# Kernel optimization log

Hardware: AMD Instinct MI355X
Metric: run time of the kernel (lower is better)

The kernel has to match this reference:

```python
import jax, jax.numpy as jnp
import numpy as np

C = 512
GROUPS = 32
EPS = 1e-6


def group_norm(x, w, b):
    # x: [B, C, H, W]
    B, Cc, H, W = x.shape
    xg = x.reshape(B, GROUPS, Cc // GROUPS, H, W)
    mean = xg.mean(axis=(2, 3, 4), keepdims=True)
    var = xg.var(axis=(2, 3, 4), keepdims=True)
    xg = (xg - mean) * jax.lax.rsqrt(var + EPS)
    x = xg.reshape(B, Cc, H, W)
    return x * w[None, :, None, None] + b[None, :, None, None]


def conv1x1(x, w, b):
    # 1x1 conv == per-pixel channel matmul; w: [Cout, Cin]
    return jnp.einsum('bchw,oc->bohw', x, w) + b[None, :, None, None]


def setup_inputs() -> dict:
    key = jax.random.key(0)
    ks = jax.random.split(key, 11)
    s = 1.0 / np.sqrt(C)
    d = {
        'x': jax.random.normal(ks[0], (2, C, 64, 64), dtype=jnp.float32),
        'gn_w': jnp.ones((C,), jnp.float32),
        'gn_b': jnp.zeros((C,), jnp.float32),
        'wq': jax.random.normal(ks[1], (C, C), jnp.float32) * s,
        'bq': jax.random.normal(ks[2], (C,), jnp.float32) * 0.01,
        'wk': jax.random.normal(ks[3], (C, C), jnp.float32) * s,
        'bk': jax.random.normal(ks[4], (C,), jnp.float32) * 0.01,
        'wv': jax.random.normal(ks[5], (C, C), jnp.float32) * s,
        'bv': jax.random.normal(ks[6], (C,), jnp.float32) * 0.01,
        'wo': jax.random.normal(ks[7], (C, C), jnp.float32) * s,
        'bo': jax.random.normal(ks[8], (C,), jnp.float32) * 0.01,
    }
    return d


def reference(x, gn_w, gn_b, wq, bq, wk, bk, wv, bv, wo, bo):
    B, Cc, H, W = x.shape
    h = group_norm(x, gn_w, gn_b)
    q = conv1x1(h, wq, bq)  # [B,C,H,W]
    k = conv1x1(h, wk, bk)
    v = conv1x1(h, wv, bv)
    N = H * W
    q = q.reshape(B, Cc, N).transpose(0, 2, 1)   # b n c
    k = k.reshape(B, Cc, N)                      # b c n
    v = v.reshape(B, Cc, N)                      # b c n
    attn = jnp.einsum('bic,bcj->bij', q, k) * (Cc ** -0.5)  # [B,N,N]
    attn = jax.nn.softmax(attn, axis=-1)
    # h_[b,c,i] = sum_j v[b,c,j] * attn[b,i,j]
    h_ = jnp.einsum('bcj,bij->bci', v, attn).reshape(B, Cc, H, W)
    h_ = conv1x1(h_, wo, bo)
    return x + h_
```

## Files before the change

### kernel.cpp

```cpp
#include <hip/hip_runtime.h>


typedef __attribute__((ext_vector_type(8))) short bf16x8;
typedef __attribute__((ext_vector_type(4))) float f32x4;
typedef unsigned short u16;
typedef unsigned int u32;

__device__ __forceinline__ u16 f2bf(float f) {
  u32 u = __builtin_bit_cast(u32, f);
  return (u16)((u + 0x7FFFu + ((u >> 16) & 1u)) >> 16);
}
__device__ __forceinline__ float bf2f(u16 u) {
  return __builtin_bit_cast(float, (u32)u << 16);
}
__device__ __forceinline__ void gll16(const void* g, void* l) {
  __builtin_amdgcn_global_load_lds((const __attribute__((address_space(1))) u32*)g,
                                   (__attribute__((address_space(3))) u32*)l, 16, 0, 0);
}

__global__ void zero_stats(float* __restrict__ stats) {
  if (threadIdx.x < 128) stats[threadIdx.x] = 0.f;
}

__global__ __launch_bounds__(256) void gn_stats(const float* __restrict__ x,
                                                float* __restrict__ stats) {
  int bg = blockIdx.x >> 3, slice = blockIdx.x & 7;
  const float4* xp = (const float4*)(x + (size_t)bg * 65536 + slice * 8192);
  int t = threadIdx.x;
  float s = 0.f, ss = 0.f;
  for (int i = t; i < 2048; i += 256) {
    float4 v = xp[i];
    s += v.x + v.y + v.z + v.w;
    ss += v.x * v.x + v.y * v.y + v.z * v.z + v.w * v.w;
  }
  for (int off = 32; off > 0; off >>= 1) {
    s += __shfl_down(s, off);
    ss += __shfl_down(ss, off);
  }
  __shared__ float rs[4], rss[4];
  if ((t & 63) == 0) { rs[t >> 6] = s; rss[t >> 6] = ss; }
  __syncthreads();
  if (t == 0) {
    atomicAdd(&stats[bg * 2 + 0], rs[0] + rs[1] + rs[2] + rs[3]);
    atomicAdd(&stats[bg * 2 + 1], rss[0] + rss[1] + rss[2] + rss[3]);
  }
}

__global__ __launch_bounds__(256) void gn_apply(
    const float* __restrict__ x, const float* __restrict__ w,
    const float* __restrict__ b, const float* __restrict__ stats,
    u16* __restrict__ ht) {
  int bg = blockIdx.x >> 3, slice = blockIdx.x & 7;
  int batch = bg >> 5, g = bg & 31;
  const float* xp = x + (size_t)bg * 65536;
  float mean = stats[bg * 2 + 0] * (1.f / 65536.f);
  float var = stats[bg * 2 + 1] * (1.f / 65536.f) - mean * mean;
  float rstd = rsqrtf(var + 1e-6f);
  float wsc[16], bsc[16];
#pragma unroll
  for (int cc = 0; cc < 16; ++cc) {
    float wv = w[g * 16 + cc];
    wsc[cc] = wv * rstd;
    bsc[cc] = b[g * 16 + cc] - mean * wsc[cc];
  }
  u16* hp = ht + (size_t)batch * 4096 * 512 + g * 16;
  int t = threadIdx.x;
  for (int n = slice * 512 + t; n < slice * 512 + 512; n += 256) {
    union { u16 pk[16]; uint4 v4[2]; } u;
#pragma unroll
    for (int cc = 0; cc < 16; ++cc)
      u.pk[cc] = f2bf(xp[cc * 4096 + n] * wsc[cc] + bsc[cc]);
    uint4* dst = (uint4*)(hp + (size_t)n * 512);
    dst[0] = u.v4[0];
    dst[1] = u.v4[1];
  }
}

__global__ __launch_bounds__(256) void wcvt_kernel(
    const float* __restrict__ wq, const float* __restrict__ wk,
    const float* __restrict__ wv, const float* __restrict__ wo,
    const float* __restrict__ bq, const float* __restrict__ bk,
    u16* __restrict__ Wqk, u16* __restrict__ Wv, u16* __restrict__ Wo,
    float* __restrict__ Bqk) {
  int i = blockIdx.x * 256 + threadIdx.x;
  Wqk[i] = f2bf(wq[i]);
  Wqk[262144 + i] = f2bf(wk[i]);
  Wv[i] = f2bf(wv[i]);
  Wo[i] = f2bf(wo[i]);
  if (i < 512) { Bqk[i] = bq[i]; Bqk[512 + i] = bk[i]; }
}

template <int BM, int BN, int MODE>
__global__ __launch_bounds__(256) void mfma_gemm(
    const u16* __restrict__ A, int sA, const u16* __restrict__ B, int sB,
    int K, const float* __restrict__ bias, const float* __restrict__ res,
    void* __restrict__ out, int ostr, float scale) {
  constexpr int TM = BM / 32, TN = BN / 32;
  constexpr int SIA = BM / 32, SIB = BN / 32;
  __shared__ char sm[(BM + BN) * 128];
  char* As = sm;
  char* Bs = sm + BM * 128;
  int t = threadIdx.x;
  int w = t >> 6, lane = t & 63, quad = lane >> 4, ln = lane & 15;
  int wm = w >> 1, wn = w & 1;
  int m0 = blockIdx.y * BM, n0 = blockIdx.x * BN;
  f32x4 acc[TM][TN] = {};

  for (int k0 = 0; k0 < K; k0 += 64) {
#pragma unroll
    for (int si = 0; si < SIA; ++si) {
      int s = (w * SIA + si) * 64 + lane;
      gll16(A + (size_t)(m0 + (s & (BM - 1))) * sA + k0 + (s / BM) * 8,
            As + (w * SIA + si) * 1024);
    }
#pragma unroll
    for (int si = 0; si < SIB; ++si) {
      int s = (w * SIB + si) * 64 + lane;
      gll16(B + (size_t)(n0 + (s & (BN - 1))) * sB + k0 + (s / BN) * 8,
            Bs + (w * SIB + si) * 1024);
    }
    __syncthreads();
#pragma unroll
    for (int ks = 0; ks < 2; ++ks) {
      bf16x8 af[TM], bfr[TN];
#pragma unroll
      for (int tm = 0; tm < TM; ++tm)
        af[tm] = *(const bf16x8*)(As + (((ks * 4 + quad) * BM) + wm * (BM / 2) + tm * 16 + ln) * 16);
#pragma unroll
      for (int tn = 0; tn < TN; ++tn)
        bfr[tn] = *(const bf16x8*)(Bs + (((ks * 4 + quad) * BN) + wn * (BN / 2) + tn * 16 + ln) * 16);
#pragma unroll
      for (int tm = 0; tm < TM; ++tm)
#pragma unroll
        for (int tn = 0; tn < TN; ++tn)
          acc[tm][tn] = __builtin_amdgcn_mfma_f32_16x16x32_bf16(af[tm], bfr[tn], acc[tm][tn], 0, 0, 0);
    }
    __syncthreads();
  }

#pragma unroll
  for (int tm = 0; tm < TM; ++tm) {
    int mb = m0 + wm * (BM / 2) + tm * 16 + quad * 4;
#pragma unroll
    for (int tn = 0; tn < TN; ++tn) {
      int n = n0 + wn * (BN / 2) + tn * 16 + ln;
      float bn = (MODE == 0) ? bias[n] : 0.f;
#pragma unroll
      for (int r = 0; r < 4; ++r) {
        int m = mb + r;
        float v = acc[tm][tn][r];
        if (MODE == 0) {
          ((u16*)out)[(size_t)m * ostr + n] = f2bf(v + bn);
        } else if (MODE == 1) {
          ((u16*)out)[(size_t)m * ostr + n] = f2bf(v + bias[m]);
        } else if (MODE == 2) {
          int bb = n >> 12, nn = n & 4095;
          size_t off = ((size_t)(bb * 512 + m)) * 4096 + nn;
          ((float*)out)[off] = v + bias[m] + res[off];
        } else if (MODE == 3) {
          ((u16*)out)[(size_t)m * ostr + n] = f2bf(v * scale);
        } else {
          ((u16*)out)[(size_t)m * ostr + n] = f2bf(v);
        }
      }
    }
  }
}

__global__ __launch_bounds__(256) void softmax_kernel(u16* __restrict__ S) {
  u16* sp = S + (size_t)blockIdx.x * 4096;
  int t = threadIdx.x;
  int w = t >> 6;
  uint4 a = ((const uint4*)sp)[t * 2];
  uint4 b = ((const uint4*)sp)[t * 2 + 1];
  u32 words[8] = {a.x, a.y, a.z, a.w, b.x, b.y, b.z, b.w};
  float v[16];
#pragma unroll
  for (int i = 0; i < 8; ++i) {
    v[2 * i] = bf2f((u16)(words[i] & 0xFFFF));
    v[2 * i + 1] = bf2f((u16)(words[i] >> 16));
  }
  float mx = v[0];
#pragma unroll
  for (int i = 1; i < 16; ++i) mx = fmaxf(mx, v[i]);
#pragma unroll
  for (int d = 1; d < 64; d <<= 1) mx = fmaxf(mx, __shfl_xor(mx, d));
  __shared__ float red[8];
  if ((t & 63) == 0) red[w] = mx;
  __syncthreads();
  mx = fmaxf(fmaxf(red[0], red[1]), fmaxf(red[2], red[3]));
  float sum = 0.f;
#pragma unroll
  for (int i = 0; i < 16; ++i) {
    v[i] = __expf(v[i] - mx);
    sum += v[i];
  }
#pragma unroll
  for (int d = 1; d < 64; d <<= 1) sum += __shfl_xor(sum, d);
  if ((t & 63) == 0) red[4 + w] = sum;
  __syncthreads();
  float inv = 1.f / (red[4] + red[5] + red[6] + red[7]);
#pragma unroll
  for (int i = 0; i < 8; ++i)
    words[i] = (u32)f2bf(v[2 * i] * inv) | ((u32)f2bf(v[2 * i + 1] * inv) << 16);
  ((uint4*)sp)[t * 2] = make_uint4(words[0], words[1], words[2], words[3]);
  ((uint4*)sp)[t * 2 + 1] = make_uint4(words[4], words[5], words[6], words[7]);
}

extern "C" void kernel_launch(void* const* d_in, const int* in_sizes, int n_in,
                              void* d_out, int out_size, void* d_ws, size_t ws_size,
                              hipStream_t stream) {
  (void)in_sizes; (void)n_in; (void)out_size; (void)ws_size;
  const float* x = (const float*)d_in[0];
  const float* gnw = (const float*)d_in[1];
  const float* gnb = (const float*)d_in[2];
  const float* wq = (const float*)d_in[3];
  const float* bq = (const float*)d_in[4];
  const float* wk = (const float*)d_in[5];
  const float* bk = (const float*)d_in[6];
  const float* wv = (const float*)d_in[7];
  const float* bv = (const float*)d_in[8];
  const float* wo = (const float*)d_in[9];
  const float* bo = (const float*)d_in[10];
  float* out = (float*)d_out;

  char* ws = (char*)d_ws;
  u16* ht  = (u16*)(ws);
  u16* AOt = (u16*)(ws);
  u16* QKt = (u16*)(ws + 8388608);
  u16* S   = (u16*)(ws + 25165824);
  u16* Wqk = (u16*)(ws + 58720256);
  u16* Wv  = (u16*)(ws + 59768832);
  u16* Wo  = (u16*)(ws + 60293120);
  u16* Vg      = (u16*)d_out;
  float* stats = (float*)((char*)d_out + 8388608);
  float* Bqk   = (float*)((char*)d_out + 8389120);

  wcvt_kernel<<<1024, 256, 0, stream>>>(wq, wk, wv, wo, bq, bk, Wqk, Wv, Wo, Bqk);
  zero_stats<<<1, 128, 0, stream>>>(stats);
  gn_stats<<<512, 256, 0, stream>>>(x, stats);
  gn_apply<<<512, 256, 0, stream>>>(x, gnw, gnb, stats, ht);
  mfma_gemm<128, 128, 0><<<dim3(8, 64), 256, 0, stream>>>(
      ht, 512, Wqk, 512, 512, Bqk, nullptr, QKt, 1024, 1.f);
  mfma_gemm<64, 128, 1><<<dim3(64, 8), 256, 0, stream>>>(
      Wv, 512, ht, 512, 512, bv, nullptr, Vg, 8192, 1.f);
  for (int b = 0; b < 2; ++b) {
    const u16* Qb = QKt + (size_t)b * 4096 * 1024;
    mfma_gemm<128, 128, 3><<<dim3(32, 32), 256, 0, stream>>>(
        Qb, 1024, Qb + 512, 1024, 512, nullptr, nullptr, S, 4096,
        0.044194173824159216f);
    softmax_kernel<<<4096, 256, 0, stream>>>(S);
    mfma_gemm<64, 64, 4><<<dim3(8, 64), 256, 0, stream>>>(
        S, 4096, Vg + (size_t)b * 4096, 8192, 4096, nullptr, nullptr,
        AOt + (size_t)b * 4096 * 512, 512, 1.f);
  }
  mfma_gemm<64, 128, 2><<<dim3(64, 8), 256, 0, stream>>>(
      Wo, 512, AOt, 512, 512, bo, x, out, 0, 1.f);
}
```

Before: 415.1 us.

## Split-K the attention-times-V GEMM into two halves with an fp32 combine kernel

The S·V GEMM (K=4096) was launched on a 512-block grid of 64x64 tiles with a long serial K loop. It now runs as split-K over blockIdx.z with two halves of K=2048, doubling the number of blocks to fill the GPU better. Each half writes fp32 partials, one into the dead Q/K region of the workspace and one into the output buffer. A new combine kernel sums them and converts to bf16. Stats and bias buffers are moved into the workspace to make room, at the cost of extra fp32 partial traffic and one more launch per batch.

```diff
diff --git a/kernel.cpp b/kernel.cpp
--- a/kernel.cpp
+++ b/kernel.cpp
@@ -104,19 +104,20 @@
   int w = t >> 6, lane = t & 63, quad = lane >> 4, ln = lane & 15;
   int wm = w >> 1, wn = w & 1;
   int m0 = blockIdx.y * BM, n0 = blockIdx.x * BN;
+  int kbase = (MODE == 5) ? blockIdx.z * K : 0;
   f32x4 acc[TM][TN] = {};
 
   for (int k0 = 0; k0 < K; k0 += 64) {
 #pragma unroll
     for (int si = 0; si < SIA; ++si) {
       int s = (w * SIA + si) * 64 + lane;
-      gll16(A + (size_t)(m0 + (s & (BM - 1))) * sA + k0 + (s / BM) * 8,
+      gll16(A + (size_t)(m0 + (s & (BM - 1))) * sA + kbase + k0 + (s / BM) * 8,
             As + (w * SIA + si) * 1024);
     }
 #pragma unroll
     for (int si = 0; si < SIB; ++si) {
       int s = (w * SIB + si) * 64 + lane;
-      gll16(B + (size_t)(n0 + (s & (BN - 1))) * sB + k0 + (s / BN) * 8,
+      gll16(B + (size_t)(n0 + (s & (BN - 1))) * sB + kbase + k0 + (s / BN) * 8,
             Bs + (w * SIB + si) * 1024);
     }
     __syncthreads();
@@ -159,8 +160,11 @@
           ((float*)out)[off] = v + bias[m] + res[off];
         } else if (MODE == 3) {
           ((u16*)out)[(size_t)m * ostr + n] = f2bf(v * scale);
+        } else if (MODE == 4) {
+          ((u16*)out)[(size_t)m * ostr + n] = f2bf(v);
         } else {
-          ((u16*)out)[(size_t)m * ostr + n] = f2bf(v);
+          float* dst = (blockIdx.z == 0) ? (float*)out : (float*)res;
+          dst[(size_t)m * ostr + n] = v;
         }
       }
     }
@@ -205,6 +209,20 @@
     words[i] = (u32)f2bf(v[2 * i] * inv) | ((u32)f2bf(v[2 * i + 1] * inv) << 16);
   ((uint4*)sp)[t * 2] = make_uint4(words[0], words[1], words[2], words[3]);
   ((uint4*)sp)[t * 2 + 1] = make_uint4(words[4], words[5], words[6], words[7]);
+}
+
+__global__ __launch_bounds__(256) void combine_kernel(
+    const float* __restrict__ P0, const float* __restrict__ P1,
+    u16* __restrict__ AOt) {
+  int i = blockIdx.x * 256 + threadIdx.x;
+  float4 a = ((const float4*)P0)[i];
+  float4 b = ((const float4*)P1)[i];
+  ushort4 o;
+  o.x = f2bf(a.x + b.x);
+  o.y = f2bf(a.y + b.y);
+  o.z = f2bf(a.z + b.z);
+  o.w = f2bf(a.w + b.w);
+  ((ushort4*)AOt)[i] = o;
 }
 
 extern "C" void kernel_launch(void* const* d_in, const int* in_sizes, int n_in,
@@ -232,9 +250,10 @@
   u16* Wqk = (u16*)(ws + 58720256);
   u16* Wv  = (u16*)(ws + 59768832);
   u16* Wo  = (u16*)(ws + 60293120);
-  u16* Vg      = (u16*)d_out;
-  float* stats = (float*)((char*)d_out + 8388608);
-  float* Bqk   = (float*)((char*)d_out + 8389120);
+  float* stats = (float*)(ws + 60817408);
+  float* Bqk   = (float*)(ws + 60817920);
+  u16* Vg   = (u16*)d_out;
+  float* P1 = (float*)((char*)d_out + 8388608);
 
   wcvt_kernel<<<1024, 256, 0, stream>>>(wq, wk, wv, wo, bq, bk, Wqk, Wv, Wo, Bqk);
   zero_stats<<<1, 128, 0, stream>>>(stats);
@@ -250,9 +269,12 @@
         Qb, 1024, Qb + 512, 1024, 512, nullptr, nullptr, S, 4096,
         0.044194173824159216f);
     softmax_kernel<<<4096, 256, 0, stream>>>(S);
-    mfma_gemm<64, 64, 4><<<dim3(8, 64), 256, 0, stream>>>(
-        S, 4096, Vg + (size_t)b * 4096, 8192, 4096, nullptr, nullptr,
-        AOt + (size_t)b * 4096 * 512, 512, 1.f);
+    float* P0 = (float*)(QKt + (size_t)b * 4096 * 1024);
+    mfma_gemm<64, 64, 5><<<dim3(8, 64, 2), 256, 0, stream>>>(
+        S, 4096, Vg + (size_t)b * 4096, 8192, 2048, nullptr,
+        (const float*)P1, P0, 512, 1.f);
+    combine_kernel<<<2048, 256, 0, stream>>>(
+        P0, P1, AOt + (size_t)b * 4096 * 512);
   }
   mfma_gemm<64, 128, 2><<<dim3(64, 8), 256, 0, stream>>>(
       Wo, 512, AOt, 512, 512, bo, x, out, 0, 1.f);
```

After: 437.1 us. +5.3%, slower.

## Split-K the attention-times-V GEMM into four partials and combine

Applied to the files above, without the earlier changes.

Replaces the 64x64-tile attn·V GEMM (K=4096, 512 blocks) with a 128x128-tile split-K version over four K slices (512 blocks), each writing a bf16 partial into spare buffers (output scratch, and the already-consumed Q/K region). A new combine kernel sums the four partials. The aim is higher per-tile reuse with larger tiles while keeping enough blocks. The cost is an extra kernel launch, extra partial traffic, and an extra bf16 rounding of the partials. Stats and biases are moved into the workspace to free room in the output buffer.

```diff
diff --git a/kernel.cpp b/kernel.cpp
--- a/kernel.cpp
+++ b/kernel.cpp
@@ -94,7 +94,8 @@
 __global__ __launch_bounds__(256) void mfma_gemm(
     const u16* __restrict__ A, int sA, const u16* __restrict__ B, int sB,
     int K, const float* __restrict__ bias, const float* __restrict__ res,
-    void* __restrict__ out, int ostr, float scale) {
+    void* __restrict__ out, int ostr, float scale,
+    u16* __restrict__ p1, u16* __restrict__ p2, u16* __restrict__ p3) {
   constexpr int TM = BM / 32, TN = BN / 32;
   constexpr int SIA = BM / 32, SIB = BN / 32;
   __shared__ char sm[(BM + BN) * 128];
@@ -104,19 +105,20 @@
   int w = t >> 6, lane = t & 63, quad = lane >> 4, ln = lane & 15;
   int wm = w >> 1, wn = w & 1;
   int m0 = blockIdx.y * BM, n0 = blockIdx.x * BN;
+  int kbase = (MODE == 5) ? blockIdx.z * K : 0;
   f32x4 acc[TM][TN] = {};
 
   for (int k0 = 0; k0 < K; k0 += 64) {
 #pragma unroll
     for (int si = 0; si < SIA; ++si) {
       int s = (w * SIA + si) * 64 + lane;
-      gll16(A + (size_t)(m0 + (s & (BM - 1))) * sA + k0 + (s / BM) * 8,
+      gll16(A + (size_t)(m0 + (s & (BM - 1))) * sA + kbase + k0 + (s / BM) * 8,
             As + (w * SIA + si) * 1024);
     }
 #pragma unroll
     for (int si = 0; si < SIB; ++si) {
       int s = (w * SIB + si) * 64 + lane;
-      gll16(B + (size_t)(n0 + (s & (BN - 1))) * sB + k0 + (s / BN) * 8,
+      gll16(B + (size_t)(n0 + (s & (BN - 1))) * sB + kbase + k0 + (s / BN) * 8,
             Bs + (w * SIB + si) * 1024);
     }
     __syncthreads();
@@ -137,6 +139,11 @@
     }
     __syncthreads();
   }
+
+  u16* pdst = nullptr;
+  if (MODE == 5)
+    pdst = (blockIdx.z == 0) ? (u16*)out : (blockIdx.z == 1) ? p1
+         : (blockIdx.z == 2) ? p2 : p3;
 
 #pragma unroll
   for (int tm = 0; tm < TM; ++tm) {
@@ -159,8 +166,10 @@
           ((float*)out)[off] = v + bias[m] + res[off];
         } else if (MODE == 3) {
           ((u16*)out)[(size_t)m * ostr + n] = f2bf(v * scale);
+        } else if (MODE == 4) {
+          ((u16*)out)[(size_t)m * ostr + n] = f2bf(v);
         } else {
-          ((u16*)out)[(size_t)m * ostr + n] = f2bf(v);
+          pdst[(size_t)m * ostr + n] = f2bf(v);
         }
       }
     }
@@ -205,6 +214,28 @@
     words[i] = (u32)f2bf(v[2 * i] * inv) | ((u32)f2bf(v[2 * i + 1] * inv) << 16);
   ((uint4*)sp)[t * 2] = make_uint4(words[0], words[1], words[2], words[3]);
   ((uint4*)sp)[t * 2 + 1] = make_uint4(words[4], words[5], words[6], words[7]);
+}
+
+__global__ __launch_bounds__(256) void combine4_kernel(
+    u16* __restrict__ P0, const u16* __restrict__ P1,
+    const u16* __restrict__ P2, const u16* __restrict__ P3) {
+  int i = blockIdx.x * 256 + threadIdx.x;
+  uint4 a = ((const uint4*)P0)[i];
+  uint4 b = ((const uint4*)P1)[i];
+  uint4 c = ((const uint4*)P2)[i];
+  uint4 d = ((const uint4*)P3)[i];
+  u32 wa[4] = {a.x, a.y, a.z, a.w}, wb[4] = {b.x, b.y, b.z, b.w};
+  u32 wc[4] = {c.x, c.y, c.z, c.w}, wd[4] = {d.x, d.y, d.z, d.w};
+  u32 wo_[4];
+#pragma unroll
+  for (int q = 0; q < 4; ++q) {
+    float lo = bf2f((u16)(wa[q] & 0xFFFF)) + bf2f((u16)(wb[q] & 0xFFFF)) +
+               bf2f((u16)(wc[q] & 0xFFFF)) + bf2f((u16)(wd[q] & 0xFFFF));
+    float hi = bf2f((u16)(wa[q] >> 16)) + bf2f((u16)(wb[q] >> 16)) +
+               bf2f((u16)(wc[q] >> 16)) + bf2f((u16)(wd[q] >> 16));
+    wo_[q] = (u32)f2bf(lo) | ((u32)f2bf(hi) << 16);
+  }
+  ((uint4*)P0)[i] = make_uint4(wo_[0], wo_[1], wo_[2], wo_[3]);
 }
 
 extern "C" void kernel_launch(void* const* d_in, const int* in_sizes, int n_in,
@@ -232,28 +263,36 @@
   u16* Wqk = (u16*)(ws + 58720256);
   u16* Wv  = (u16*)(ws + 59768832);
   u16* Wo  = (u16*)(ws + 60293120);
-  u16* Vg      = (u16*)d_out;
-  float* stats = (float*)((char*)d_out + 8388608);
-  float* Bqk   = (float*)((char*)d_out + 8389120);
+  float* stats = (float*)(ws + 60817408);
+  float* Bqk   = (float*)(ws + 60817920);
+  u16* Vg  = (u16*)d_out;
+  u16* P1g = (u16*)((char*)d_out + 8388608);
+  u16* P2g = (u16*)((char*)d_out + 12582912);
 
   wcvt_kernel<<<1024, 256, 0, stream>>>(wq, wk, wv, wo, bq, bk, Wqk, Wv, Wo, Bqk);
   zero_stats<<<1, 128, 0, stream>>>(stats);
   gn_stats<<<512, 256, 0, stream>>>(x, stats);
   gn_apply<<<512, 256, 0, stream>>>(x, gnw, gnb, stats, ht);
   mfma_gemm<128, 128, 0><<<dim3(8, 64), 256, 0, stream>>>(
-      ht, 512, Wqk, 512, 512, Bqk, nullptr, QKt, 1024, 1.f);
+      ht, 512, Wqk, 512, 512, Bqk, nullptr, QKt, 1024, 1.f,
+      nullptr, nullptr, nullptr);
   mfma_gemm<64, 128, 1><<<dim3(64, 8), 256, 0, stream>>>(
-      Wv, 512, ht, 512, 512, bv, nullptr, Vg, 8192, 1.f);
+      Wv, 512, ht, 512, 512, bv, nullptr, Vg, 8192, 1.f,
+      nullptr, nullptr, nullptr);
   for (int b = 0; b < 2; ++b) {
     const u16* Qb = QKt + (size_t)b * 4096 * 1024;
     mfma_gemm<128, 128, 3><<<dim3(32, 32), 256, 0, stream>>>(
         Qb, 1024, Qb + 512, 1024, 512, nullptr, nullptr, S, 4096,
-        0.044194173824159216f);
+        0.044194173824159216f, nullptr, nullptr, nullptr);
     softmax_kernel<<<4096, 256, 0, stream>>>(S);
-    mfma_gemm<64, 64, 4><<<dim3(8, 64), 256, 0, stream>>>(
-        S, 4096, Vg + (size_t)b * 4096, 8192, 4096, nullptr, nullptr,
-        AOt + (size_t)b * 4096 * 512, 512, 1.f);
+    u16* P0 = AOt + (size_t)b * 4096 * 512;
+    u16* P3 = QKt + (size_t)b * 4096 * 1024;
+    mfma_gemm<128, 128, 5><<<dim3(4, 32, 4), 256, 0, stream>>>(
+        S, 4096, Vg + (size_t)b * 4096, 8192, 1024, nullptr, nullptr,
+        P0, 512, 1.f, P1g, P2g, P3);
+    combine4_kernel<<<1024, 256, 0, stream>>>(P0, P1g, P2g, P3);
   }
   mfma_gemm<64, 128, 2><<<dim3(64, 8), 256, 0, stream>>>(
-      Wo, 512, AOt, 512, 512, bo, x, out, 0, 1.f);
-}
+      Wo, 512, AOt, 512, 512, bo, x, out, 0, 1.f,
+      nullptr, nullptr, nullptr);
+}
```

After: 373.3 us. 10.1% less time.
